# Performance work log

Measured on AMD Instinct MI355X. Metric: run time of the kernel, lower is better.

## Reference

```python
import jax, jax.numpy as jnp
import numpy as np

EMBED = 768
HIDDEN = 4 * EMBED
TEMPERATURE = 1.0
LN_EPS = 1e-5


def setup_inputs() -> dict:
    key = jax.random.key(0)
    ks = jax.random.split(key, 10)
    s = 1.0 / np.sqrt(EMBED)
    sh = 1.0 / np.sqrt(HIDDEN)
    return {
        "x": jax.random.normal(ks[0], (32, 577, EMBED), dtype=jnp.float32),
        "Wq": jax.random.normal(ks[1], (EMBED, EMBED), dtype=jnp.float32) * s,
        "Wk": jax.random.normal(ks[2], (EMBED, EMBED), dtype=jnp.float32) * s,
        "Wv": jax.random.normal(ks[3], (EMBED, EMBED), dtype=jnp.float32) * s,
        "ln1_g": jnp.ones((EMBED,), jnp.float32),
        "ln1_b": jnp.zeros((EMBED,), jnp.float32),
        "ln2_g": jnp.ones((EMBED,), jnp.float32),
        "ln2_b": jnp.zeros((EMBED,), jnp.float32),
        "W1": jax.random.normal(ks[4], (EMBED, HIDDEN), dtype=jnp.float32) * s,
        "b1": jnp.zeros((HIDDEN,), jnp.float32),
        "W2": jax.random.normal(ks[5], (HIDDEN, EMBED), dtype=jnp.float32) * sh,
        "b2": jnp.zeros((EMBED,), jnp.float32),
    }


def layer_norm(x, g, b):
    mu = jnp.mean(x, axis=-1, keepdims=True)
    var = jnp.mean(jnp.square(x - mu), axis=-1, keepdims=True)
    return (x - mu) * jax.lax.rsqrt(var + LN_EPS) * g + b


def l2_attention(h, Wq, Wk, Wv):
    # h: [b, s, d]
    Q = h @ Wq
    K = h @ Wk
    V = h @ Wv
    q_sq = jnp.sum(Q * Q, axis=-1, keepdims=True)          # [b, s, 1]
    k_sq = jnp.sum(K * K, axis=-1, keepdims=True)          # [b, s, 1]
    qk = jnp.einsum('bqd,bkd->bqk', Q, K)                  # [b, s, s]
    l2_sq = q_sq + jnp.swapaxes(k_sq, -2, -1) - 2.0 * qk
    attn = jax.nn.softmax(-l2_sq / TEMPERATURE, axis=-1)
    return jnp.einsum('bqk,bkd->bqd', attn, V)


def reference(x, Wq, Wk, Wv, ln1_g, ln1_b, ln2_g, ln2_b, W1, b1, W2, b2):
    x = x + l2_attention(layer_norm(x, ln1_g, ln1_b), Wq, Wk, Wv)
    h = layer_norm(x, ln2_g, ln2_b)
    h = jax.nn.gelu(h @ W1 + b1, approximate=False) @ W2 + b2
    return x + h
```

## Files before the change

### kernel.cpp

```cpp
#include <hip/hip_runtime.h>

#define EMBED 768
#define HIDDEN 3072
#define SEQ 577
#define BATCH 32
#define ROWS (BATCH*SEQ)
#define KPAD 608
#define SLD 640

typedef __attribute__((ext_vector_type(4))) float f32x4;
typedef __attribute__((ext_vector_type(8))) __bf16 bf16x8;
typedef unsigned int __attribute__((address_space(1))) as1_u32;
typedef unsigned int __attribute__((address_space(3))) as3_u32;

__device__ __forceinline__ unsigned short f2b(float f) {
    unsigned int u = __float_as_uint(f);
    u = u + 0x7FFFu + ((u >> 16) & 1u);
    return (unsigned short)(u >> 16);
}
__device__ __forceinline__ float b2f(unsigned short s) {
    return __uint_as_float(((unsigned int)s) << 16);
}
__device__ __forceinline__ void gld16(const unsigned short* g, unsigned short* l) {
    __builtin_amdgcn_global_load_lds((const as1_u32*)g, (as3_u32*)l, 16, 0, 0);
}

__device__ __forceinline__ void tile_coords(int& row0, int& col0) {
    int nx = gridDim.x;
    int lin = blockIdx.y * nx + blockIdx.x;
    if (gridDim.z == 1) {
        int nwg = nx * gridDim.y;
        int q = nwg >> 3, r = nwg & 7;
        int xcd = lin & 7, blk = lin >> 3;
        lin = (xcd < r ? xcd * (q + 1) : r * (q + 1) + (xcd - r) * q) + blk;
    }
    row0 = (lin / nx) * 128;
    col0 = (lin % nx) * 128;
}

__global__ void ln_kernel(const float* __restrict__ x, const float* __restrict__ g,
                          const float* __restrict__ b, unsigned short* __restrict__ o) {
    int row = blockIdx.x;
    const float* xr = x + (size_t)row * EMBED;
    int t = threadIdx.x;
    float v0 = xr[t], v1 = xr[t + 256], v2 = xr[t + 512];
    float s = v0 + v1 + v2;
    float ss = v0 * v0 + v1 * v1 + v2 * v2;
#pragma unroll
    for (int d = 32; d; d >>= 1) { s += __shfl_down(s, d); ss += __shfl_down(ss, d); }
    __shared__ float rs[4], rss[4];
    if ((t & 63) == 0) { rs[t >> 6] = s; rss[t >> 6] = ss; }
    __syncthreads();
    s = rs[0] + rs[1] + rs[2] + rs[3];
    ss = rss[0] + rss[1] + rss[2] + rss[3];
    float mu = s * (1.0f / EMBED);
    float var = ss * (1.0f / EMBED) - mu * mu;
    float rstd = rsqrtf(var + 1e-5f);
    unsigned short* orow = o + (size_t)row * EMBED;
    orow[t]       = f2b((v0 - mu) * rstd * g[t]       + b[t]);
    orow[t + 256] = f2b((v1 - mu) * rstd * g[t + 256] + b[t + 256]);
    orow[t + 512] = f2b((v2 - mu) * rstd * g[t + 512] + b[t + 512]);
}

__global__ void ln_split_kernel(const float* __restrict__ x, const float* __restrict__ g,
                                const float* __restrict__ b, unsigned short* __restrict__ oh,
                                unsigned short* __restrict__ ol) {
    int row = blockIdx.x;
    const float* xr = x + (size_t)row * EMBED;
    int t = threadIdx.x;
    float v0 = xr[t], v1 = xr[t + 256], v2 = xr[t + 512];
    float s = v0 + v1 + v2;
    float ss = v0 * v0 + v1 * v1 + v2 * v2;
#pragma unroll
    for (int d = 32; d; d >>= 1) { s += __shfl_down(s, d); ss += __shfl_down(ss, d); }
    __shared__ float rs[4], rss[4];
    if ((t & 63) == 0) { rs[t >> 6] = s; rss[t >> 6] = ss; }
    __syncthreads();
    s = rs[0] + rs[1] + rs[2] + rs[3];
    ss = rss[0] + rss[1] + rss[2] + rss[3];
    float mu = s * (1.0f / EMBED);
    float var = ss * (1.0f / EMBED) - mu * mu;
    float rstd = rsqrtf(var + 1e-5f);
    size_t base = (size_t)row * EMBED;
#pragma unroll
    for (int i = 0; i < 3; i++) {
        int d = t + 256 * i;
        float v = (i == 0 ? v0 : (i == 1 ? v1 : v2));
        float y = (v - mu) * rstd * g[d] + b[d];
        unsigned short h = f2b(y);
        oh[base + d] = h;
        ol[base + d] = f2b(y - b2f(h));
    }
}

__global__ void ksq_kernel(const unsigned short* __restrict__ qh,
                           const unsigned short* __restrict__ ql, float* __restrict__ ksq) {
    int row = blockIdx.x;
    int t = threadIdx.x;
    size_t base = (size_t)row * 1536 + EMBED;
    float s = 0.f;
#pragma unroll
    for (int i = 0; i < 3; i++) {
        int d = t + 256 * i;
        float k = b2f(qh[base + d]) + b2f(ql[base + d]);
        s += k * k;
    }
#pragma unroll
    for (int d = 32; d; d >>= 1) s += __shfl_down(s, d);
    __shared__ float rs[4];
    if ((t & 63) == 0) rs[t >> 6] = s;
    __syncthreads();
    if (t == 0) ksq[row] = rs[0] + rs[1] + rs[2] + rs[3];
}

__global__ void softmax_kernel(const float* __restrict__ S, unsigned short* __restrict__ P) {
    int r = blockIdx.x;
    int t = threadIdx.x;
    const float* sr = S + (size_t)r * SLD;
    float v0 = sr[t];
    float v1 = sr[t + 256];
    float v2 = (t + 512 < SEQ) ? sr[t + 512] : -3.0e38f;
    float m = fmaxf(v0, fmaxf(v1, v2));
#pragma unroll
    for (int d = 32; d; d >>= 1) m = fmaxf(m, __shfl_down(m, d));
    __shared__ float rm[4];
    if ((t & 63) == 0) rm[t >> 6] = m;
    __syncthreads();
    m = fmaxf(fmaxf(rm[0], rm[1]), fmaxf(rm[2], rm[3]));
    float e0 = expf(v0 - m);
    float e1 = expf(v1 - m);
    float e2 = (t + 512 < SEQ) ? expf(v2 - m) : 0.0f;
    float s = e0 + e1 + e2;
#pragma unroll
    for (int d = 32; d; d >>= 1) s += __shfl_down(s, d);
    __shared__ float rsum[4];
    if ((t & 63) == 0) rsum[t >> 6] = s;
    __syncthreads();
    float inv = 1.0f / (rsum[0] + rsum[1] + rsum[2] + rsum[3]);
    unsigned short* pr = P + (size_t)r * KPAD;
    pr[t]       = f2b(e0 * inv);
    pr[t + 256] = f2b(e1 * inv);
    if (t + 512 < KPAD) pr[t + 512] = f2b(e2 * inv);
}

__global__ void wt_kernel(const float* __restrict__ in, unsigned short* __restrict__ out,
                          int K, int N, int outRowOff, int outLd) {
    __shared__ float tile[32][33];
    int n0 = blockIdx.x * 32, k0 = blockIdx.y * 32;
    int tx = threadIdx.x, ty = threadIdx.y;
#pragma unroll
    for (int i = 0; i < 4; i++)
        tile[ty + 8 * i][tx] = in[(size_t)(k0 + ty + 8 * i) * N + (n0 + tx)];
    __syncthreads();
#pragma unroll
    for (int i = 0; i < 4; i++)
        out[(size_t)(outRowOff + n0 + ty + 8 * i) * outLd + (k0 + tx)] = f2b(tile[tx][ty + 8 * i]);
}

__global__ void wt_split_kernel(const float* __restrict__ in, unsigned short* __restrict__ oh,
                                unsigned short* __restrict__ ol,
                                int K, int N, int outRowOff, int outLd) {
    __shared__ float tile[32][33];
    int n0 = blockIdx.x * 32, k0 = blockIdx.y * 32;
    int tx = threadIdx.x, ty = threadIdx.y;
#pragma unroll
    for (int i = 0; i < 4; i++)
        tile[ty + 8 * i][tx] = in[(size_t)(k0 + ty + 8 * i) * N + (n0 + tx)];
    __syncthreads();
#pragma unroll
    for (int i = 0; i < 4; i++) {
        float v = tile[tx][ty + 8 * i];
        unsigned short h = f2b(v);
        size_t idx = (size_t)(outRowOff + n0 + ty + 8 * i) * outLd + (k0 + tx);
        oh[idx] = h;
        ol[idx] = f2b(v - b2f(h));
    }
}

__global__ void vt_kernel(const unsigned short* __restrict__ vbuf, unsigned short* __restrict__ vt) {
    int z = blockIdx.z;
    int d0 = blockIdx.x * 32, c0 = blockIdx.y * 32;
    __shared__ unsigned short tile[32][33];
    int tx = threadIdx.x, ty = threadIdx.y;
#pragma unroll
    for (int i = 0; i < 4; i++) {
        int c = c0 + ty + 8 * i;
        tile[ty + 8 * i][tx] = (c < SEQ) ? vbuf[((size_t)z * SEQ + c) * EMBED + d0 + tx]
                                         : (unsigned short)0;
    }
    __syncthreads();
#pragma unroll
    for (int i = 0; i < 4; i++) {
        int d = d0 + ty + 8 * i, c = c0 + tx;
        vt[(size_t)z * EMBED * KPAD + (size_t)d * KPAD + c] = tile[tx][ty + 8 * i];
    }
}

template <int EPI>
__global__ __launch_bounds__(256, 2) void gemm_bt(
    const unsigned short* __restrict__ A, int lda, long long sA,
    const unsigned short* __restrict__ B, int ldb, long long sB,
    int M, int N, int K,
    void* __restrict__ C, int ldc, long long sC,
    const float* __restrict__ E, long long sE) {
    __shared__ unsigned short As[2][4096];
    __shared__ unsigned short Bs[2][4096];
    int z = blockIdx.z;
    A += (size_t)z * sA;
    B += (size_t)z * sB;
    int row0, col0;
    tile_coords(row0, col0);
    int t = threadIdx.x, l = t & 63, w = t >> 6;
    int wr = w >> 1, wc = w & 1;

    f32x4 acc[4][4] = {};

    int srow = t >> 2;
    int sblk = t & 3;
    int kboff = (sblk ^ ((srow >> 1) & 3)) * 8;

    auto stage = [&](int buf, int kt) {
#pragma unroll
        for (int c = 0; c < 2; ++c) {
            int ar = row0 + c * 64 + srow; ar = ar < M ? ar : M - 1;
            gld16(A + (size_t)ar * lda + kt + kboff, &As[buf][c * 2048 + t * 8]);
            int br = col0 + c * 64 + srow; br = br < N ? br : N - 1;
            gld16(B + (size_t)br * ldb + kt + kboff, &Bs[buf][c * 2048 + t * 8]);
        }
    };
    auto compute = [&](int buf) {
        bf16x8 af[4], bfr[4];
        int kb = l >> 4;
#pragma unroll
        for (int m = 0; m < 4; m++) {
            int r = wr * 64 + m * 16 + (l & 15);
            int blk = kb ^ ((r >> 1) & 3);
            af[m] = *reinterpret_cast<const bf16x8*>(&As[buf][r * 32 + blk * 8]);
        }
#pragma unroll
        for (int n = 0; n < 4; n++) {
            int r = wc * 64 + n * 16 + (l & 15);
            int blk = kb ^ ((r >> 1) & 3);
            bfr[n] = *reinterpret_cast<const bf16x8*>(&Bs[buf][r * 32 + blk * 8]);
        }
#pragma unroll
        for (int m = 0; m < 4; m++)
#pragma unroll
            for (int n = 0; n < 4; n++)
                acc[m][n] = __builtin_amdgcn_mfma_f32_16x16x32_bf16(af[m], bfr[n], acc[m][n], 0, 0, 0);
    };

    stage(0, 0);
    asm volatile("s_waitcnt vmcnt(0)" ::: "memory");
    __builtin_amdgcn_s_barrier();
    __builtin_amdgcn_sched_barrier(0);
    int cur = 0;
    for (int kt = 32; kt < K; kt += 32) {
        stage(cur ^ 1, kt);
        compute(cur);
        asm volatile("s_waitcnt vmcnt(0)" ::: "memory");
        __builtin_amdgcn_s_barrier();
        __builtin_amdgcn_sched_barrier(0);
        cur ^= 1;
    }
    compute(cur);

    int rbase = row0 + wr * 64 + (l >> 4) * 4;
    int cbase = col0 + wc * 64 + (l & 15);
#pragma unroll
    for (int m = 0; m < 4; m++) {
#pragma unroll
        for (int n = 0; n < 4; n++) {
            int col = cbase + n * 16;
            if (col >= N) continue;
#pragma unroll
            for (int j = 0; j < 4; j++) {
                int row = rbase + m * 16 + j;
                if (row >= M) continue;
                float v = acc[m][n][j];
                size_t oidx = (size_t)z * sC + (size_t)row * ldc + col;
                if (EPI == 0) {
                    ((unsigned short*)C)[oidx] = f2b(v);
                } else if (EPI == 2) {
                    ((float*)C)[oidx] = E[oidx] + v;
                } else if (EPI == 3) {
                    float xx = v + E[col];
                    float g = 0.5f * xx * (1.0f + erff(xx * 0.70710678118654752f));
                    ((unsigned short*)C)[oidx] = f2b(g);
                } else if (EPI == 4) {
                    ((float*)C)[oidx] += v + E[col];
                }
            }
        }
    }
}

template <int EPI>
__global__ __launch_bounds__(256, 2) void gemm_hp(
    const unsigned short* __restrict__ Ah, const unsigned short* __restrict__ Al, int lda, long long sA,
    const unsigned short* __restrict__ Bh, const unsigned short* __restrict__ Bl, int ldb, long long sB,
    int M, int N, int K,
    void* __restrict__ C, int ldc, long long sC, long long planeOff,
    const float* __restrict__ E, long long sE) {
    __shared__ unsigned short Ash[4096], Asl[4096], Bsh[4096], Bsl[4096];
    int z = blockIdx.z;
    Ah += (size_t)z * sA; Al += (size_t)z * sA;
    Bh += (size_t)z * sB; Bl += (size_t)z * sB;
    int row0, col0;
    tile_coords(row0, col0);
    int t = threadIdx.x, l = t & 63, w = t >> 6;
    int wr = w >> 1, wc = w & 1;

    f32x4 acc[4][4] = {};

    int srow = t >> 2;
    int sblk = t & 3;
    int kboff = (sblk ^ ((srow >> 1) & 3)) * 8;

    for (int kt = 0; kt < K; kt += 32) {
#pragma unroll
        for (int c = 0; c < 2; ++c) {
            int ar = row0 + c * 64 + srow; ar = ar < M ? ar : M - 1;
            size_t aoff = (size_t)ar * lda + kt + kboff;
            gld16(Ah + aoff, Ash + c * 2048 + t * 8);
            gld16(Al + aoff, Asl + c * 2048 + t * 8);
            int br = col0 + c * 64 + srow; br = br < N ? br : N - 1;
            size_t boff = (size_t)br * ldb + kt + kboff;
            gld16(Bh + boff, Bsh + c * 2048 + t * 8);
            gld16(Bl + boff, Bsl + c * 2048 + t * 8);
        }
        __syncthreads();
        int kb = l >> 4;
        bf16x8 afh[4], afl[4], bfh[4], bfl[4];
#pragma unroll
        for (int m = 0; m < 4; m++) {
            int r = wr * 64 + m * 16 + (l & 15);
            int blk = kb ^ ((r >> 1) & 3);
            afh[m] = *reinterpret_cast<const bf16x8*>(&Ash[r * 32 + blk * 8]);
            afl[m] = *reinterpret_cast<const bf16x8*>(&Asl[r * 32 + blk * 8]);
        }
#pragma unroll
        for (int n = 0; n < 4; n++) {
            int r = wc * 64 + n * 16 + (l & 15);
            int blk = kb ^ ((r >> 1) & 3);
            bfh[n] = *reinterpret_cast<const bf16x8*>(&Bsh[r * 32 + blk * 8]);
            bfl[n] = *reinterpret_cast<const bf16x8*>(&Bsl[r * 32 + blk * 8]);
        }
#pragma unroll
        for (int m = 0; m < 4; m++)
#pragma unroll
            for (int n = 0; n < 4; n++) {
                acc[m][n] = __builtin_amdgcn_mfma_f32_16x16x32_bf16(afh[m], bfh[n], acc[m][n], 0, 0, 0);
                acc[m][n] = __builtin_amdgcn_mfma_f32_16x16x32_bf16(afh[m], bfl[n], acc[m][n], 0, 0, 0);
                acc[m][n] = __builtin_amdgcn_mfma_f32_16x16x32_bf16(afl[m], bfh[n], acc[m][n], 0, 0, 0);
            }
        __syncthreads();
    }

    int rbase = row0 + wr * 64 + (l >> 4) * 4;
    int cbase = col0 + wc * 64 + (l & 15);
#pragma unroll
    for (int m = 0; m < 4; m++) {
#pragma unroll
        for (int n = 0; n < 4; n++) {
            int col = cbase + n * 16;
            if (col >= N) continue;
#pragma unroll
            for (int j = 0; j < 4; j++) {
                int row = rbase + m * 16 + j;
                if (row >= M) continue;
                float v = acc[m][n][j];
                size_t oidx = (size_t)z * sC + (size_t)row * ldc + col;
                if (EPI == 0) {
                    unsigned short h = f2b(v);
                    ((unsigned short*)C)[oidx] = h;
                    ((unsigned short*)C)[oidx + planeOff] = f2b(v - b2f(h));
                } else if (EPI == 1) {
                    ((float*)C)[oidx] = 2.0f * v - E[(size_t)z * sE + col];
                }
            }
        }
    }
}

extern "C" void kernel_launch(void* const* d_in, const int* in_sizes, int n_in,
                              void* d_out, int out_size, void* d_ws, size_t ws_size,
                              hipStream_t stream) {
    const float* x   = (const float*)d_in[0];
    const float* Wq  = (const float*)d_in[1];
    const float* Wk  = (const float*)d_in[2];
    const float* Wv  = (const float*)d_in[3];
    const float* g1  = (const float*)d_in[4];
    const float* be1 = (const float*)d_in[5];
    const float* g2  = (const float*)d_in[6];
    const float* be2 = (const float*)d_in[7];
    const float* W1  = (const float*)d_in[8];
    const float* bb1 = (const float*)d_in[9];
    const float* W2  = (const float*)d_in[10];
    const float* bb2 = (const float*)d_in[11];
    float* out = (float*)d_out;

    char* ws = (char*)d_ws;
    size_t off = 0;
    auto alloc = [&](size_t bytes) -> char* {
        char* p = ws + off;
        off += (bytes + 255) & ~(size_t)255;
        return p;
    };
    unsigned short* wqkTh = (unsigned short*)alloc((size_t)1536 * EMBED * 2);
    unsigned short* wqkTl = (unsigned short*)alloc((size_t)1536 * EMBED * 2);
    unsigned short* wvT   = (unsigned short*)alloc((size_t)EMBED * EMBED * 2);
    unsigned short* w1T   = (unsigned short*)alloc((size_t)HIDDEN * EMBED * 2);
    unsigned short* w2T   = (unsigned short*)alloc((size_t)EMBED * HIDDEN * 2);
    float*          ksqb  = (float*)alloc((size_t)ROWS * 4);
    char* regB = alloc((size_t)ROWS * HIDDEN * 2);
    char* regC = alloc((size_t)2 * ROWS * EMBED * 2);
    unsigned short* vbuf  = (unsigned short*)alloc((size_t)ROWS * EMBED * 2);
    unsigned short* vtb   = (unsigned short*)alloc((size_t)BATCH * EMBED * KPAD * 2);
    unsigned short* Pbuf  = (unsigned short*)alloc((size_t)ROWS * KPAD * 2);
    if (off > ws_size) return;

    unsigned short* qkh  = (unsigned short*)regB;
    unsigned short* qkl  = qkh + (size_t)ROWS * 1536;
    unsigned short* hid  = (unsigned short*)regB;
    unsigned short* h1h  = (unsigned short*)regC;
    unsigned short* h1l  = h1h + (size_t)ROWS * EMBED;
    float*          Sbuf = (float*)regC;
    unsigned short* h2   = (unsigned short*)regC;

    dim3 b256(256), bT(32, 8);

    wt_split_kernel<<<dim3(24, 24), bT, 0, stream>>>(Wq, wqkTh, wqkTl, EMBED, EMBED, 0, EMBED);
    wt_split_kernel<<<dim3(24, 24), bT, 0, stream>>>(Wk, wqkTh, wqkTl, EMBED, EMBED, EMBED, EMBED);
    wt_kernel<<<dim3(24, 24), bT, 0, stream>>>(Wv, wvT, EMBED, EMBED, 0, EMBED);
    wt_kernel<<<dim3(96, 24), bT, 0, stream>>>(W1, w1T, EMBED, HIDDEN, 0, EMBED);
    wt_kernel<<<dim3(24, 96), bT, 0, stream>>>(W2, w2T, HIDDEN, EMBED, 0, HIDDEN);

    ln_split_kernel<<<ROWS, b256, 0, stream>>>(x, g1, be1, h1h, h1l);

    gemm_hp<0><<<dim3(12, 145, 1), b256, 0, stream>>>(
        h1h, h1l, EMBED, 0, wqkTh, wqkTl, EMBED, 0,
        ROWS, 1536, EMBED, qkh, 1536, 0, (long long)ROWS * 1536, nullptr, 0);

    gemm_bt<0><<<dim3(6, 145, 1), b256, 0, stream>>>(
        h1h, EMBED, 0, wvT, EMBED, 0, ROWS, EMBED, EMBED, vbuf, EMBED, 0, nullptr, 0);

    ksq_kernel<<<ROWS, b256, 0, stream>>>(qkh, qkl, ksqb);

    gemm_hp<1><<<dim3(5, 5, 32), b256, 0, stream>>>(
        qkh, qkl, 1536, (long long)SEQ * 1536, qkh + EMBED, qkl + EMBED, 1536, (long long)SEQ * 1536,
        SEQ, SEQ, EMBED, Sbuf, SLD, (long long)SEQ * SLD, 0, ksqb, SEQ);

    softmax_kernel<<<ROWS, b256, 0, stream>>>(Sbuf, Pbuf);

    vt_kernel<<<dim3(24, 19, 32), bT, 0, stream>>>(vbuf, vtb);

    gemm_bt<2><<<dim3(6, 5, 32), b256, 0, stream>>>(
        Pbuf, KPAD, (long long)SEQ * KPAD, vtb, KPAD, (long long)EMBED * KPAD,
        SEQ, EMBED, KPAD, out, EMBED, (long long)SEQ * EMBED, x, (long long)SEQ * EMBED);

    ln_kernel<<<ROWS, b256, 0, stream>>>(out, g2, be2, h2);

    gemm_bt<3><<<dim3(24, 145, 1), b256, 0, stream>>>(
        h2, EMBED, 0, w1T, EMBED, 0, ROWS, HIDDEN, EMBED, hid, HIDDEN, 0, bb1, 0);

    gemm_bt<4><<<dim3(6, 145, 1), b256, 0, stream>>>(
        hid, HIDDEN, 0, w2T, HIDDEN, 0, ROWS, EMBED, HIDDEN, out, EMBED, 0, bb2, 0);
}
```

Before: 893.2 us.

## Add 256x256-tile 512-thread GEMM with interleaved staging for V and MLP projections

Adds a new bf16 GEMM kernel using 256x256 output tiles, 8 waves per block, and a two-deep LDS buffer. Global-to-LDS loads for the next tiles are issued between halves of the MFMA work, separated by barriers and with raised wave priority during MFMA bursts. The V projection and both MLP GEMMs now use this kernel instead of the 128x128 one, aiming for more operand reuse per loaded byte and better overlap of loads with compute. The larger tiles mean fewer blocks and more partial tiles at the M edge, and they raise register and LDS pressure per block.

New measurement: 1.067 ms. 19.4% more time.

```diff
diff --git a/kernel.cpp b/kernel.cpp
--- a/kernel.cpp
+++ b/kernel.cpp
@@ -25,7 +25,10 @@
     __builtin_amdgcn_global_load_lds((const as1_u32*)g, (as3_u32*)l, 16, 0, 0);
 }
 
-__device__ __forceinline__ void tile_coords(int& row0, int& col0) {
+#define BARRIER() do { asm volatile("" ::: "memory"); __builtin_amdgcn_s_barrier(); \
+                       __builtin_amdgcn_sched_barrier(0); } while (0)
+
+__device__ __forceinline__ int swz_lin() {
     int nx = gridDim.x;
     int lin = blockIdx.y * nx + blockIdx.x;
     if (gridDim.z == 1) {
@@ -34,8 +37,7 @@
         int xcd = lin & 7, blk = lin >> 3;
         lin = (xcd < r ? xcd * (q + 1) : r * (q + 1) + (xcd - r) * q) + blk;
     }
-    row0 = (lin / nx) * 128;
-    col0 = (lin % nx) * 128;
+    return lin;
 }
 
 __global__ void ln_kernel(const float* __restrict__ x, const float* __restrict__ g,
@@ -193,6 +195,110 @@
     for (int i = 0; i < 4; i++) {
         int d = d0 + ty + 8 * i, c = c0 + tx;
         vt[(size_t)z * EMBED * KPAD + (size_t)d * KPAD + c] = tile[tx][ty + 8 * i];
+    }
+}
+
+template <int EPI>
+__global__ __launch_bounds__(512, 2) void gemm256(
+    const unsigned short* __restrict__ A, int lda,
+    const unsigned short* __restrict__ B, int ldb,
+    int M, int N, int K,
+    void* __restrict__ C, int ldc,
+    const float* __restrict__ E) {
+    __shared__ unsigned short As[2][2][4096];
+    __shared__ unsigned short Bs[2][2][4096];
+    int nx = gridDim.x;
+    int lin = swz_lin();
+    int row0 = (lin / nx) * 256, col0 = (lin % nx) * 256;
+    int t = threadIdx.x, l = t & 63, w = t >> 6;
+    int wr = w >> 2, wc = w & 3;
+
+    f32x4 acc[8][4] = {};
+
+    int srow = t >> 2, sblk = t & 3;
+    int skb = (sblk ^ ((srow >> 1) & 3)) * 8;
+
+    auto stageH = [&](int buf, int kt, int h) {
+        if (h < 2) {
+            int ar = row0 + h * 128 + srow; ar = ar < M ? ar : M - 1;
+            gld16(A + (size_t)ar * lda + kt + skb, &As[buf][h][t * 8]);
+        } else {
+            int br = col0 + (h - 2) * 128 + srow; br = br < N ? br : N - 1;
+            gld16(B + (size_t)br * ldb + kt + skb, &Bs[buf][h - 2][t * 8]);
+        }
+    };
+    int NT = K >> 5;
+    stageH(0, 0, 0); stageH(0, 0, 1); stageH(0, 0, 2); stageH(0, 0, 3);
+    stageH(1, 32, 0); stageH(1, 32, 1); stageH(1, 32, 2);
+    asm volatile("s_waitcnt vmcnt(3)" ::: "memory");
+    __builtin_amdgcn_s_barrier();
+    __builtin_amdgcn_sched_barrier(0);
+
+    int l15 = l & 15, kb = l >> 4;
+    for (int tt = 0; tt < NT; ++tt) {
+        int cur = tt & 1;
+        int kt1 = (tt + 1 < NT ? tt + 1 : NT - 1) * 32;
+        int kt2 = (tt + 2 < NT ? tt + 2 : NT - 1) * 32;
+        bf16x8 af[8], bfv[4];
+#pragma unroll
+        for (int mf = 0; mf < 8; mf++) {
+            int r = mf * 16 + l15; int blk = kb ^ ((r >> 1) & 3);
+            af[mf] = *reinterpret_cast<const bf16x8*>(&As[cur][wr][r * 32 + blk * 8]);
+        }
+#pragma unroll
+        for (int nf = 0; nf < 4; nf++) {
+            int r = (wc & 1) * 64 + nf * 16 + l15; int blk = kb ^ ((r >> 1) & 3);
+            bfv[nf] = *reinterpret_cast<const bf16x8*>(&Bs[cur][wc >> 1][r * 32 + blk * 8]);
+        }
+        stageH(cur ^ 1, kt1, 3);
+        BARRIER();
+        __builtin_amdgcn_s_setprio(1);
+#pragma unroll
+        for (int mf = 0; mf < 4; mf++)
+#pragma unroll
+            for (int nf = 0; nf < 4; nf++)
+                acc[mf][nf] = __builtin_amdgcn_mfma_f32_16x16x32_bf16(af[mf], bfv[nf], acc[mf][nf], 0, 0, 0);
+        __builtin_amdgcn_s_setprio(0);
+        BARRIER();
+        stageH(cur, kt2, 0); stageH(cur, kt2, 1); stageH(cur, kt2, 2);
+        BARRIER();
+        __builtin_amdgcn_s_setprio(1);
+#pragma unroll
+        for (int mf = 4; mf < 8; mf++)
+#pragma unroll
+            for (int nf = 0; nf < 4; nf++)
+                acc[mf][nf] = __builtin_amdgcn_mfma_f32_16x16x32_bf16(af[mf], bfv[nf], acc[mf][nf], 0, 0, 0);
+        __builtin_amdgcn_s_setprio(0);
+        BARRIER();
+        asm volatile("s_waitcnt vmcnt(3)" ::: "memory");
+    }
+    asm volatile("s_waitcnt vmcnt(0)" ::: "memory");
+
+    int rbase = row0 + wr * 128 + (l >> 4) * 4;
+    int cbase = col0 + wc * 64 + l15;
+#pragma unroll
+    for (int mf = 0; mf < 8; mf++) {
+#pragma unroll
+        for (int nf = 0; nf < 4; nf++) {
+            int col = cbase + nf * 16;
+            if (col >= N) continue;
+#pragma unroll
+            for (int j = 0; j < 4; j++) {
+                int row = rbase + mf * 16 + j;
+                if (row >= M) continue;
+                float v = acc[mf][nf][j];
+                size_t oidx = (size_t)row * ldc + col;
+                if (EPI == 0) {
+                    ((unsigned short*)C)[oidx] = f2b(v);
+                } else if (EPI == 3) {
+                    float xx = v + E[col];
+                    float g = 0.5f * xx * (1.0f + erff(xx * 0.70710678118654752f));
+                    ((unsigned short*)C)[oidx] = f2b(g);
+                } else if (EPI == 4) {
+                    ((float*)C)[oidx] += v + E[col];
+                }
+            }
+        }
     }
 }
 
@@ -208,8 +314,9 @@
     int z = blockIdx.z;
     A += (size_t)z * sA;
     B += (size_t)z * sB;
-    int row0, col0;
-    tile_coords(row0, col0);
+    int nx = gridDim.x;
+    int lin = swz_lin();
+    int row0 = (lin / nx) * 128, col0 = (lin % nx) * 128;
     int t = threadIdx.x, l = t & 63, w = t >> 6;
     int wr = w >> 1, wc = w & 1;
 
@@ -279,16 +386,8 @@
                 if (row >= M) continue;
                 float v = acc[m][n][j];
                 size_t oidx = (size_t)z * sC + (size_t)row * ldc + col;
-                if (EPI == 0) {
-                    ((unsigned short*)C)[oidx] = f2b(v);
-                } else if (EPI == 2) {
+                if (EPI == 2) {
                     ((float*)C)[oidx] = E[oidx] + v;
-                } else if (EPI == 3) {
-                    float xx = v + E[col];
-                    float g = 0.5f * xx * (1.0f + erff(xx * 0.70710678118654752f));
-                    ((unsigned short*)C)[oidx] = f2b(g);
-                } else if (EPI == 4) {
-                    ((float*)C)[oidx] += v + E[col];
                 }
             }
         }
@@ -306,8 +405,9 @@
     int z = blockIdx.z;
     Ah += (size_t)z * sA; Al += (size_t)z * sA;
     Bh += (size_t)z * sB; Bl += (size_t)z * sB;
-    int row0, col0;
-    tile_coords(row0, col0);
+    int nx = gridDim.x;
+    int lin = swz_lin();
+    int row0 = (lin / nx) * 128, col0 = (lin % nx) * 128;
     int t = threadIdx.x, l = t & 63, w = t >> 6;
     int wr = w >> 1, wc = w & 1;
 
@@ -428,7 +528,7 @@
     float*          Sbuf = (float*)regC;
     unsigned short* h2   = (unsigned short*)regC;
 
-    dim3 b256(256), bT(32, 8);
+    dim3 b256(256), b512(512), bT(32, 8);
 
     wt_split_kernel<<<dim3(24, 24), bT, 0, stream>>>(Wq, wqkTh, wqkTl, EMBED, EMBED, 0, EMBED);
     wt_split_kernel<<<dim3(24, 24), bT, 0, stream>>>(Wk, wqkTh, wqkTl, EMBED, EMBED, EMBED, EMBED);
@@ -442,8 +542,8 @@
         h1h, h1l, EMBED, 0, wqkTh, wqkTl, EMBED, 0,
         ROWS, 1536, EMBED, qkh, 1536, 0, (long long)ROWS * 1536, nullptr, 0);
 
-    gemm_bt<0><<<dim3(6, 145, 1), b256, 0, stream>>>(
-        h1h, EMBED, 0, wvT, EMBED, 0, ROWS, EMBED, EMBED, vbuf, EMBED, 0, nullptr, 0);
+    gemm256<0><<<dim3(3, 73), b512, 0, stream>>>(
+        h1h, EMBED, wvT, EMBED, ROWS, EMBED, EMBED, vbuf, EMBED, nullptr);
 
     ksq_kernel<<<ROWS, b256, 0, stream>>>(qkh, qkl, ksqb);
 
@@ -461,9 +561,9 @@
 
     ln_kernel<<<ROWS, b256, 0, stream>>>(out, g2, be2, h2);
 
-    gemm_bt<3><<<dim3(24, 145, 1), b256, 0, stream>>>(
-        h2, EMBED, 0, w1T, EMBED, 0, ROWS, HIDDEN, EMBED, hid, HIDDEN, 0, bb1, 0);
-
-    gemm_bt<4><<<dim3(6, 145, 1), b256, 0, stream>>>(
-        hid, HIDDEN, 0, w2T, HIDDEN, 0, ROWS, EMBED, HIDDEN, out, EMBED, 0, bb2, 0);
-}
+    gemm256<3><<<dim3(12, 73), b512, 0, stream>>>(
+        h2, EMBED, w1T, EMBED, ROWS, HIDDEN, EMBED, hid, HIDDEN, bb1);
+
+    gemm256<4><<<dim3(3, 73), b512, 0, stream>>>(
+        hid, HIDDEN, w2T, HIDDEN, ROWS, EMBED, HIDDEN, out, EMBED, bb2);
+}
```
